# Kernel optimization log

Measured on AMD Instinct MI355X. Metric: run time of the kernel, lower is better.

Reference implementation:

```python
import jax, jax.numpy as jnp
import numpy as np

TEMPERATURE = 0.1
EPS = 1e-12  # matches torch F.normalize default eps


def setup_inputs() -> dict:
    key = jax.random.key(0)
    k1, k2 = jax.random.split(key)
    B, D = 4096, 512
    features1 = jax.random.normal(k1, (B, D), dtype=jnp.float32)
    features2 = jax.random.normal(k2, (B, D), dtype=jnp.float32)
    return {"features1": features1, "features2": features2}


def _l2_normalize(x, axis=1):
    norm = jnp.linalg.norm(x, axis=axis, keepdims=True)
    return x / jnp.maximum(norm, EPS)


def reference(features1, features2):
    B = features1.shape[0]
    f1 = _l2_normalize(features1)
    f2 = _l2_normalize(features2)
    features = jnp.concatenate([f1, f2], axis=0)  # (2B, D)
    sim = jnp.matmul(features, features.T) / TEMPERATURE  # (2B, 2B)
    # mask self-similarity on the diagonal with -inf
    diag = jnp.eye(2 * B, dtype=bool)
    sim = jnp.where(diag, -jnp.inf, sim)
    # positive pair labels: row i pairs with i+B (first half) / i-B (second half)
    labels = jnp.concatenate([jnp.arange(B) + B, jnp.arange(B)], axis=0)
    log_probs = jax.nn.log_softmax(sim, axis=-1)  # (2B, 2B)
    nll = -jnp.take_along_axis(log_probs, labels[:, None], axis=1)[:, 0]
    return jnp.mean(nll)
```

## Files before the change

kernel.cpp:

```cpp
#include <hip/hip_runtime.h>

#define NROWS 8192
#define HALF_N 4096
#define DIM 512
#define INV_T 10.0f
#define NRB 64
#define NBLOCKS 2080

typedef __attribute__((ext_vector_type(4))) float f32x4;

__device__ __forceinline__ void async16(const void* g, void* l) {
  __builtin_amdgcn_global_load_lds(
      (const __attribute__((address_space(1))) unsigned int*)g,
      (__attribute__((address_space(3))) unsigned int*)l, 16, 0, 0);
}

__global__ __launch_bounds__(256) void norm_cast_k(
    const float* __restrict__ f1, const float* __restrict__ f2,
    unsigned char* __restrict__ Fn, float* __restrict__ rowsum) {
  int wave = threadIdx.x >> 6;
  int lane = threadIdx.x & 63;
  int row = blockIdx.x * 4 + wave;
  const float* src = (row < HALF_N) ? (f1 + (size_t)row * DIM)
                                    : (f2 + (size_t)(row - HALF_N) * DIM);
  const float4* p = reinterpret_cast<const float4*>(src + lane * 8);
  float4 v0 = p[0];
  float4 v1 = p[1];
  float ss = v0.x*v0.x + v0.y*v0.y + v0.z*v0.z + v0.w*v0.w
           + v1.x*v1.x + v1.y*v1.y + v1.z*v1.z + v1.w*v1.w;
  #pragma unroll
  for (int off = 1; off < 64; off <<= 1) ss += __shfl_xor(ss, off);
  float scale = 1.0f / fmaxf(sqrtf(ss), 1e-12f);
  int lo = __builtin_amdgcn_cvt_pk_fp8_f32(v0.x * scale, v0.y * scale, 0, false);
  lo = __builtin_amdgcn_cvt_pk_fp8_f32(v0.z * scale, v0.w * scale, lo, true);
  int hi = __builtin_amdgcn_cvt_pk_fp8_f32(v1.x * scale, v1.y * scale, 0, false);
  hi = __builtin_amdgcn_cvt_pk_fp8_f32(v1.z * scale, v1.w * scale, hi, true);
  *reinterpret_cast<int2*>(Fn + (size_t)row * DIM + lane * 8) = make_int2(lo, hi);
  if (lane == 0) rowsum[row] = 0.0f;
}

__global__ __launch_bounds__(256, 3) void sym_gemm_k(
    const unsigned char* __restrict__ Fn, float* __restrict__ rowsum,
    float* __restrict__ pairsim) {
  int bx = blockIdx.x;
  int gbx = (bx & 7) * (NBLOCKS / 8) + (bx >> 3);
  int rb = 0, rem = gbx;
  while (rem >= NRB - rb) { rem -= NRB - rb; ++rb; }
  const int cb = rb + rem;
  const int row0 = rb * 128, col0 = cb * 128;

  const int tid = threadIdx.x;
  const int wave = tid >> 6;
  const int lane = tid & 63;
  const int quad = lane >> 4;
  const int colid = lane & 15;
  const int wr0 = (wave >> 1) * 64;
  const int wc0 = (wave & 1) * 64;

  __shared__ __align__(16) unsigned char Alds[128 * 64];
  __shared__ __align__(16) unsigned char Blds[128 * 64];
  __shared__ float redrow[128];
  __shared__ float redcol[128];

  if (tid < 128) { redrow[tid] = 0.0f; redcol[tid] = 0.0f; }

  const unsigned char* srcA[2]; const unsigned char* srcB[2];
  unsigned char* dstA[2]; unsigned char* dstB[2];
  #pragma unroll
  for (int seg = 0; seg < 2; ++seg) {
    int inst = wave + seg * 4;
    int r = inst * 16 + (lane >> 2);
    int c = (lane & 3) ^ ((r >> 1) & 3);
    srcA[seg] = Fn + (size_t)(row0 + r) * DIM + c * 16;
    srcB[seg] = Fn + (size_t)(col0 + r) * DIM + c * 16;
    dstA[seg] = Alds + inst * 1024;
    dstB[seg] = Blds + inst * 1024;
  }

  const unsigned char* afp[4][2]; const unsigned char* bfp[4][2];
  #pragma unroll
  for (int t = 0; t < 4; ++t) {
    int ra = wr0 + t * 16 + colid;
    int rc = wc0 + t * 16 + colid;
    #pragma unroll
    for (int s = 0; s < 2; ++s) {
      int c16 = s * 2 + (quad >> 1);
      afp[t][s] = Alds + ra * 64 + ((c16 ^ ((ra >> 1) & 3)) << 4) + (quad & 1) * 8;
      bfp[t][s] = Blds + rc * 64 + ((c16 ^ ((rc >> 1) & 3)) << 4) + (quad & 1) * 8;
    }
  }

  f32x4 acc[4][4];
  #pragma unroll
  for (int t = 0; t < 4; ++t)
    #pragma unroll
    for (int u = 0; u < 4; ++u) acc[t][u] = (f32x4){0.f, 0.f, 0.f, 0.f};

  for (int kc = 0; kc < 8; ++kc) {
    __syncthreads();
    const size_t ko = (size_t)kc * 64;
    #pragma unroll
    for (int seg = 0; seg < 2; ++seg) {
      async16(srcA[seg] + ko, dstA[seg]);
      async16(srcB[seg] + ko, dstB[seg]);
    }
    __syncthreads();

    #pragma unroll
    for (int s = 0; s < 2; ++s) {
      long af[4], bf[4];
      #pragma unroll
      for (int t = 0; t < 4; ++t) af[t] = *reinterpret_cast<const long*>(afp[t][s]);
      #pragma unroll
      for (int u = 0; u < 4; ++u) bf[u] = *reinterpret_cast<const long*>(bfp[u][s]);
      #pragma unroll
      for (int t = 0; t < 4; ++t)
        #pragma unroll
        for (int u = 0; u < 4; ++u)
          acc[t][u] = __builtin_amdgcn_mfma_f32_16x16x32_fp8_fp8(af[t], bf[u], acc[t][u], 0, 0, 0);
    }
  }

  float re[4][4];
  float ce[4];
  #pragma unroll
  for (int t = 0; t < 4; ++t)
    #pragma unroll
    for (int r = 0; r < 4; ++r) re[t][r] = 0.0f;
  #pragma unroll
  for (int u = 0; u < 4; ++u) ce[u] = 0.0f;

  #pragma unroll
  for (int t = 0; t < 4; ++t) {
    #pragma unroll
    for (int u = 0; u < 4; ++u) {
      f32x4 a = acc[t][u];
      const int gc = col0 + wc0 + u * 16 + colid;
      #pragma unroll
      for (int r = 0; r < 4; ++r) {
        int grow = row0 + wr0 + t * 16 + quad * 4 + r;
        float sim = a[r] * INV_T;
        float e = (gc > grow) ? __expf(sim) : 0.0f;
        re[t][r] += e;
        ce[u] += e;
        if (gc == grow + HALF_N && grow < HALF_N) {
          pairsim[grow] = sim;
          pairsim[gc] = sim;
        }
      }
    }
  }

  #pragma unroll
  for (int t = 0; t < 4; ++t)
    #pragma unroll
    for (int r = 0; r < 4; ++r) {
      float v = re[t][r];
      v += __shfl_xor(v, 1); v += __shfl_xor(v, 2);
      v += __shfl_xor(v, 4); v += __shfl_xor(v, 8);
      if (colid == 0) atomicAdd(&redrow[wr0 + t * 16 + quad * 4 + r], v);
    }
  #pragma unroll
  for (int u = 0; u < 4; ++u) {
    float v = ce[u];
    v += __shfl_xor(v, 16); v += __shfl_xor(v, 32);
    if (lane < 16) atomicAdd(&redcol[wc0 + u * 16 + colid], v);
  }
  __syncthreads();
  if (tid < 128) atomicAdd(&rowsum[row0 + tid], redrow[tid]);
  else           atomicAdd(&rowsum[col0 + tid - 128], redcol[tid - 128]);
}

__global__ __launch_bounds__(1024) void finalize_k(
    const float* __restrict__ rowsum, const float* __restrict__ pairsim,
    float* __restrict__ out) {
  float local = 0.0f;
  for (int i = threadIdx.x; i < NROWS; i += 1024)
    local += logf(rowsum[i]) - pairsim[i];
  #pragma unroll
  for (int off = 1; off < 64; off <<= 1) local += __shfl_xor(local, off);
  __shared__ float red[16];
  int wave = threadIdx.x >> 6;
  int lane = threadIdx.x & 63;
  if (lane == 0) red[wave] = local;
  __syncthreads();
  if (threadIdx.x == 0) {
    float s = 0.0f;
    #pragma unroll
    for (int w = 0; w < 16; ++w) s += red[w];
    out[0] = s * (1.0f / (float)NROWS);
  }
}

extern "C" void kernel_launch(void* const* d_in, const int* in_sizes, int n_in,
                              void* d_out, int out_size, void* d_ws, size_t ws_size,
                              hipStream_t stream) {
  const float* f1 = (const float*)d_in[0];
  const float* f2 = (const float*)d_in[1];
  unsigned char* Fn = (unsigned char*)d_ws;
  float* rowsum = (float*)((char*)d_ws + (size_t)NROWS * DIM);
  float* pairsim = rowsum + NROWS;
  float* out = (float*)d_out;

  norm_cast_k<<<NROWS / 4, 256, 0, stream>>>(f1, f2, Fn, rowsum);
  sym_gemm_k<<<NBLOCKS, 256, 0, stream>>>(Fn, rowsum, pairsim);
  finalize_k<<<1, 1024, 0, stream>>>(rowsum, pairsim, out);
}
```

Measured before the change: 111.2 us.

## Use gfx950 16x16x128 scaled FP8 MFMA with 128-byte K chunks

Replaces the 16x16x32 FP8 MFMA with the gfx950 scaled 16x16x128 f8f6f4 MFMA, using unit scales (exponent 127). The K chunk per LDS stage doubles to 128 bytes, which halves the number of k-iterations and barrier pairs. The LDS tiles, global-to-LDS load mapping and XOR swizzle are reworked for 128-byte rows, and each fragment is now read as two 16-byte loads. LDS use doubles, which may reduce occupancy, and the new operand layout has to match what the instruction expects for the results to be correct.

```diff
diff --git a/kernel.cpp b/kernel.cpp
--- a/kernel.cpp
+++ b/kernel.cpp
@@ -8,6 +8,8 @@
 #define NBLOCKS 2080
 
 typedef __attribute__((ext_vector_type(4))) float f32x4;
+typedef __attribute__((ext_vector_type(4))) int i32x4;
+typedef __attribute__((ext_vector_type(8))) int i32x8;
 
 __device__ __forceinline__ void async16(const void* g, void* l) {
   __builtin_amdgcn_global_load_lds(
@@ -57,37 +59,38 @@
   const int wr0 = (wave >> 1) * 64;
   const int wc0 = (wave & 1) * 64;
 
-  __shared__ __align__(16) unsigned char Alds[128 * 64];
-  __shared__ __align__(16) unsigned char Blds[128 * 64];
+  __shared__ __align__(16) unsigned char Alds[128 * 128];
+  __shared__ __align__(16) unsigned char Blds[128 * 128];
   __shared__ float redrow[128];
   __shared__ float redcol[128];
 
   if (tid < 128) { redrow[tid] = 0.0f; redcol[tid] = 0.0f; }
 
-  const unsigned char* srcA[2]; const unsigned char* srcB[2];
-  unsigned char* dstA[2]; unsigned char* dstB[2];
-  #pragma unroll
-  for (int seg = 0; seg < 2; ++seg) {
+  const unsigned char* srcA[4]; const unsigned char* srcB[4];
+  unsigned char* dstA[4]; unsigned char* dstB[4];
+  #pragma unroll
+  for (int seg = 0; seg < 4; ++seg) {
     int inst = wave + seg * 4;
-    int r = inst * 16 + (lane >> 2);
-    int c = (lane & 3) ^ ((r >> 1) & 3);
+    int r = inst * 8 + (lane >> 3);
+    int c = (lane & 7) ^ (lane >> 3);
     srcA[seg] = Fn + (size_t)(row0 + r) * DIM + c * 16;
     srcB[seg] = Fn + (size_t)(col0 + r) * DIM + c * 16;
     dstA[seg] = Alds + inst * 1024;
     dstB[seg] = Blds + inst * 1024;
   }
 
-  const unsigned char* afp[4][2]; const unsigned char* bfp[4][2];
+  const unsigned char* afp0[4]; const unsigned char* afp1[4];
+  const unsigned char* bfp0[4]; const unsigned char* bfp1[4];
   #pragma unroll
   for (int t = 0; t < 4; ++t) {
     int ra = wr0 + t * 16 + colid;
     int rc = wc0 + t * 16 + colid;
-    #pragma unroll
-    for (int s = 0; s < 2; ++s) {
-      int c16 = s * 2 + (quad >> 1);
-      afp[t][s] = Alds + ra * 64 + ((c16 ^ ((ra >> 1) & 3)) << 4) + (quad & 1) * 8;
-      bfp[t][s] = Blds + rc * 64 + ((c16 ^ ((rc >> 1) & 3)) << 4) + (quad & 1) * 8;
-    }
+    int ca0 = (2 * quad) ^ (ra & 7);
+    int cb0 = (2 * quad) ^ (rc & 7);
+    afp0[t] = Alds + ra * 128 + ca0 * 16;
+    afp1[t] = Alds + ra * 128 + (ca0 ^ 1) * 16;
+    bfp0[t] = Blds + rc * 128 + cb0 * 16;
+    bfp1[t] = Blds + rc * 128 + (cb0 ^ 1) * 16;
   }
 
   f32x4 acc[4][4];
@@ -96,29 +99,37 @@
     #pragma unroll
     for (int u = 0; u < 4; ++u) acc[t][u] = (f32x4){0.f, 0.f, 0.f, 0.f};
 
-  for (int kc = 0; kc < 8; ++kc) {
+  for (int kc = 0; kc < 4; ++kc) {
     __syncthreads();
-    const size_t ko = (size_t)kc * 64;
-    #pragma unroll
-    for (int seg = 0; seg < 2; ++seg) {
+    const size_t ko = (size_t)kc * 128;
+    #pragma unroll
+    for (int seg = 0; seg < 4; ++seg) {
       async16(srcA[seg] + ko, dstA[seg]);
       async16(srcB[seg] + ko, dstB[seg]);
     }
     __syncthreads();
 
-    #pragma unroll
-    for (int s = 0; s < 2; ++s) {
-      long af[4], bf[4];
+    i32x8 af[4], bf[4];
+    #pragma unroll
+    for (int t = 0; t < 4; ++t) {
+      i32x4 lo = *reinterpret_cast<const i32x4*>(afp0[t]);
+      i32x4 hi = *reinterpret_cast<const i32x4*>(afp1[t]);
+      af[t] = (i32x8){lo.x, lo.y, lo.z, lo.w, hi.x, hi.y, hi.z, hi.w};
+    }
+    #pragma unroll
+    for (int u = 0; u < 4; ++u) {
+      i32x4 lo = *reinterpret_cast<const i32x4*>(bfp0[u]);
+      i32x4 hi = *reinterpret_cast<const i32x4*>(bfp1[u]);
+      bf[u] = (i32x8){lo.x, lo.y, lo.z, lo.w, hi.x, hi.y, hi.z, hi.w};
+    }
+    #pragma unroll
+    for (int t = 0; t < 4; ++t)
       #pragma unroll
-      for (int t = 0; t < 4; ++t) af[t] = *reinterpret_cast<const long*>(afp[t][s]);
-      #pragma unroll
-      for (int u = 0; u < 4; ++u) bf[u] = *reinterpret_cast<const long*>(bfp[u][s]);
-      #pragma unroll
-      for (int t = 0; t < 4; ++t)
-        #pragma unroll
-        for (int u = 0; u < 4; ++u)
-          acc[t][u] = __builtin_amdgcn_mfma_f32_16x16x32_fp8_fp8(af[t], bf[u], acc[t][u], 0, 0, 0);
-    }
+      for (int u = 0; u < 4; ++u)
+        acc[t][u] = __builtin_amdgcn_mfma_scale_f32_16x16x128_f8f6f4(
+            af[t], bf[u], acc[t][u],
+            0 , 0 ,
+            0, 127 , 0, 127 );
   }
 
   float re[4][4];
```

After: 248.8 us. 124% more time.
